# Performance work log

Hardware: AMD Instinct MI355X
Metric: run time of the kernel (lower is better)

Reference implementation:

```python
import jax, jax.numpy as jnp
import numpy as np

def setup_inputs() -> dict:
    key = jax.random.key(0)
    k1, k2, k3, k4 = jax.random.split(key, 4)
    B = 128
    x1 = jax.random.normal(k1, (B, 2048, 7, 7), dtype=jnp.float32)
    x2 = jax.random.normal(k2, (B, 2048, 7, 7), dtype=jnp.float32)
    x3 = jax.random.normal(k3, (B, 2048, 7, 7), dtype=jnp.float32)
    W = jax.random.normal(k4, (14, 2048), dtype=jnp.float32) * 0.02
    b = jnp.zeros((14,), dtype=jnp.float32)
    return {"x1": x1, "x2": x2, "x3": x3, "W": W, "b": b}

def reference(x1, x2, x3, W, b):
    B = x1.shape[0]
    # (B, 2048, 49)
    x1r = x1.reshape(B, 2048, 49)
    x2r = x2.reshape(B, 2048, 49)
    x3r = x3.reshape(B, 2048, 49)
    # diagonal of matmul(x3, x1^T) == per-row dot product over the 49-dim axis
    # (avoids materializing the (B,2048,2048) intermediate)
    d31 = jnp.einsum('bnc,bnc->bn', x3r, x1r)[..., None]  # (B, 2048, 1)
    d32 = jnp.einsum('bnc,bnc->bn', x3r, x2r)[..., None]
    # softmax over last (singleton) axis -> all ones, kept for faithfulness
    d31 = jax.nn.softmax(d31, axis=-1)
    d32 = jax.nn.softmax(d32, axis=-1)
    h = x1r + x1r * d31 + x2r * d32  # (B, 2048, 49)
    # AvgPool2d(7) on (B,2048,7,7) == mean over the 49 spatial positions
    feats = jnp.mean(h, axis=-1)  # (B, 2048)
    # dropout omitted (deterministic eval); fc
    logits = feats @ W.T + b  # (B, 14)
    return (logits, feats)
```

## Files before the change

kernel.cpp:

```cpp
#include <hip/hip_runtime.h>


#define FC_B 128
#define FC_N 2048
#define FC_J 14
#define TILE_ROWS 64
#define TILE_F (TILE_ROWS * 49)
#define TILE_V (TILE_F / 4)
#define TPB 4
#define RPB (TPB * TILE_ROWS)
#define NBLK (FC_B * FC_N / RPB)
#define BPB (FC_N / RPB)

__global__ __launch_bounds__(256) void fused_kernel(
    const float* __restrict__ x1, const float* __restrict__ x2,
    const float* __restrict__ W,
    float* __restrict__ feats, float* __restrict__ part)
{
    const int tid = threadIdx.x;
    __shared__ float buf[2][TILE_F];
    __shared__ __align__(16) float sf[RPB];

    const float4* q1 = (const float4*)x1 + (size_t)blockIdx.x * (TPB * TILE_V);
    const float4* q2 = (const float4*)x2 + (size_t)blockIdx.x * (TPB * TILE_V);

    float4 r1a, r1b, r1c, r2a, r2b, r2c, tl1, tl2;

    r1a = q1[tid]; r1b = q1[tid + 256]; r1c = q1[tid + 512];
    r2a = q2[tid]; r2b = q2[tid + 256]; r2c = q2[tid + 512];
    if (tid < 16) { tl1 = q1[768 + tid]; tl2 = q2[768 + tid]; }

    const int row = tid >> 2;
    const int tt = tid & 3;

    #pragma unroll
    for (int t = 0; t < TPB; ++t) {
        float4* smv = (float4*)buf[t & 1];
        float4 w0, w1, w2;
        w0.x = 2.f*r1a.x + r2a.x; w0.y = 2.f*r1a.y + r2a.y;
        w0.z = 2.f*r1a.z + r2a.z; w0.w = 2.f*r1a.w + r2a.w;
        w1.x = 2.f*r1b.x + r2b.x; w1.y = 2.f*r1b.y + r2b.y;
        w1.z = 2.f*r1b.z + r2b.z; w1.w = 2.f*r1b.w + r2b.w;
        w2.x = 2.f*r1c.x + r2c.x; w2.y = 2.f*r1c.y + r2c.y;
        w2.z = 2.f*r1c.z + r2c.z; w2.w = 2.f*r1c.w + r2c.w;
        smv[tid] = w0; smv[tid + 256] = w1; smv[tid + 512] = w2;
        if (tid < 16) {
            float4 wt;
            wt.x = 2.f*tl1.x + tl2.x; wt.y = 2.f*tl1.y + tl2.y;
            wt.z = 2.f*tl1.z + tl2.z; wt.w = 2.f*tl1.w + tl2.w;
            smv[768 + tid] = wt;
        }

        if (t < TPB - 1) {
            const float4* Q1 = q1 + (t + 1) * TILE_V;
            const float4* Q2 = q2 + (t + 1) * TILE_V;
            r1a = Q1[tid]; r1b = Q1[tid + 256]; r1c = Q1[tid + 512];
            r2a = Q2[tid]; r2b = Q2[tid + 256]; r2c = Q2[tid + 512];
            if (tid < 16) { tl1 = Q1[768 + tid]; tl2 = Q2[768 + tid]; }
        }

        asm volatile("s_waitcnt lgkmcnt(0)" ::: "memory");
        __builtin_amdgcn_s_barrier();

        const float* rp = buf[t & 1] + row * 49;
        float v = 0.f;
        #pragma unroll
        for (int k = 0; k < 12; ++k)
            v += rp[tt + 4 * k];
        if (tt == 0) v += rp[48];
        v += __shfl_xor(v, 1, 4);
        v += __shfl_xor(v, 2, 4);
        if (tt == 0) sf[t * TILE_ROWS + row] = v * (1.0f / 49.0f);
    }

    asm volatile("s_waitcnt lgkmcnt(0)" ::: "memory");
    __builtin_amdgcn_s_barrier();

    if (tid < 64)
        ((float4*)(feats + (size_t)blockIdx.x * RPB))[tid] =
            ((const float4*)sf)[tid];

    if (tid < 224) {
        const int j = tid >> 4;
        const int s = tid & 15;
        const int bb = blockIdx.x >> 3;
        const int blkin = blockIdx.x & (BPB - 1);
        const float* wrow = W + j * FC_N + blkin * RPB;
        float acc = 0.f;
        #pragma unroll
        for (int k = 0; k < 16; ++k)
            acc += sf[s + 16 * k] * wrow[s + 16 * k];
        acc += __shfl_xor(acc, 1, 16);
        acc += __shfl_xor(acc, 2, 16);
        acc += __shfl_xor(acc, 4, 16);
        acc += __shfl_xor(acc, 8, 16);
        if (s == 0)
            part[((bb * FC_J + j) << 3) + blkin] = acc;
    }
}

__global__ __launch_bounds__(256) void gather_kernel(const float* __restrict__ part,
                                                     const float* __restrict__ bias,
                                                     float* __restrict__ logits) {
    const int idx = blockIdx.x * 256 + threadIdx.x;
    if (idx >= FC_B * FC_J) return;
    const float4 p0 = ((const float4*)(part + ((size_t)idx << 3)))[0];
    const float4 p1 = ((const float4*)(part + ((size_t)idx << 3)))[1];
    logits[idx] = p0.x + p0.y + p0.z + p0.w
                + p1.x + p1.y + p1.z + p1.w + bias[idx % FC_J];
}

extern "C" void kernel_launch(void* const* d_in, const int* in_sizes, int n_in,
                              void* d_out, int out_size, void* d_ws, size_t ws_size,
                              hipStream_t stream) {
    const float* x1 = (const float*)d_in[0];
    const float* x2 = (const float*)d_in[1];
    const float* W = (const float*)d_in[3];
    const float* bias = (const float*)d_in[4];

    float* out = (float*)d_out;
    float* logits = out;
    float* feats = out + FC_B * FC_J;

    float* part = (float*)d_ws;

    fused_kernel<<<NBLK, 256, 0, stream>>>(x1, x2, W, feats, part);
    gather_kernel<<<(FC_B * FC_J + 255) / 256, 256, 0, stream>>>(part, bias, logits);
}
```

Measured before the change: 22.56 us.

## Give each wavefront a private sub-tile pipeline to drop block-wide barriers

Each of the four wavefronts now owns its own contiguous 64-row chunk and double-buffered LDS region. It processes that chunk in 16-row sub-tiles with a register prefetch issued before the current tile is consumed. The per-tile block barrier is replaced by a wave-local LDS wait, leaving a single __syncthreads before the FC epilogue. This is meant to remove barrier stalls and let waves stream memory independently, at the cost of more registers for the doubled prefetch buffers.

Measured after the change: 22.84 us. No clear change (+1.2%).

```diff
diff --git a/kernel.cpp b/kernel.cpp
--- a/kernel.cpp
+++ b/kernel.cpp
@@ -4,11 +4,12 @@
 #define FC_B 128
 #define FC_N 2048
 #define FC_J 14
-#define TILE_ROWS 64
-#define TILE_F (TILE_ROWS * 49)
-#define TILE_V (TILE_F / 4)
-#define TPB 4
-#define RPB (TPB * TILE_ROWS)
+#define SUBT 4
+#define SUB_ROWS 16
+#define SUB_F (SUB_ROWS * 49)
+#define SUB_V (SUB_F / 4)
+#define WCHUNK_V (SUBT * SUB_V)
+#define RPB 256
 #define NBLK (FC_B * FC_N / RPB)
 #define BPB (FC_N / RPB)
 
@@ -18,63 +19,67 @@
     float* __restrict__ feats, float* __restrict__ part)
 {
     const int tid = threadIdx.x;
-    __shared__ float buf[2][TILE_F];
+    const int w = tid >> 6;
+    const int lane = tid & 63;
+    __shared__ float buf[4][2][SUB_F];
     __shared__ __align__(16) float sf[RPB];
 
-    const float4* q1 = (const float4*)x1 + (size_t)blockIdx.x * (TPB * TILE_V);
-    const float4* q2 = (const float4*)x2 + (size_t)blockIdx.x * (TPB * TILE_V);
+    const float4* q1 = (const float4*)x1
+                     + (size_t)blockIdx.x * (RPB * 49 / 4) + w * WCHUNK_V;
+    const float4* q2 = (const float4*)x2
+                     + (size_t)blockIdx.x * (RPB * 49 / 4) + w * WCHUNK_V;
 
-    float4 r1a, r1b, r1c, r2a, r2b, r2c, tl1, tl2;
+    float4 a0[2], a1[2], a2[2], at[2], c0[2], c1[2], c2[2], ct[2];
 
-    r1a = q1[tid]; r1b = q1[tid + 256]; r1c = q1[tid + 512];
-    r2a = q2[tid]; r2b = q2[tid + 256]; r2c = q2[tid + 512];
-    if (tid < 16) { tl1 = q1[768 + tid]; tl2 = q2[768 + tid]; }
+    a0[0] = q1[lane]; a1[0] = q1[lane + 64]; a2[0] = q1[lane + 128];
+    c0[0] = q2[lane]; c1[0] = q2[lane + 64]; c2[0] = q2[lane + 128];
+    if (lane < 4) { at[0] = q1[192 + lane]; ct[0] = q2[192 + lane]; }
 
-    const int row = tid >> 2;
-    const int tt = tid & 3;
+    const int r = lane >> 2;
+    const int t4 = lane & 3;
 
     #pragma unroll
-    for (int t = 0; t < TPB; ++t) {
-        float4* smv = (float4*)buf[t & 1];
-        float4 w0, w1, w2;
-        w0.x = 2.f*r1a.x + r2a.x; w0.y = 2.f*r1a.y + r2a.y;
-        w0.z = 2.f*r1a.z + r2a.z; w0.w = 2.f*r1a.w + r2a.w;
-        w1.x = 2.f*r1b.x + r2b.x; w1.y = 2.f*r1b.y + r2b.y;
-        w1.z = 2.f*r1b.z + r2b.z; w1.w = 2.f*r1b.w + r2b.w;
-        w2.x = 2.f*r1c.x + r2c.x; w2.y = 2.f*r1c.y + r2c.y;
-        w2.z = 2.f*r1c.z + r2c.z; w2.w = 2.f*r1c.w + r2c.w;
-        smv[tid] = w0; smv[tid + 256] = w1; smv[tid + 512] = w2;
-        if (tid < 16) {
-            float4 wt;
-            wt.x = 2.f*tl1.x + tl2.x; wt.y = 2.f*tl1.y + tl2.y;
-            wt.z = 2.f*tl1.z + tl2.z; wt.w = 2.f*tl1.w + tl2.w;
-            smv[768 + tid] = wt;
+    for (int s = 0; s < SUBT; ++s) {
+        const int cur = s & 1, nxt = cur ^ 1;
+
+        if (s < SUBT - 1) {
+            const float4* Q1 = q1 + (s + 1) * SUB_V;
+            const float4* Q2 = q2 + (s + 1) * SUB_V;
+            a0[nxt] = Q1[lane]; a1[nxt] = Q1[lane + 64]; a2[nxt] = Q1[lane + 128];
+            c0[nxt] = Q2[lane]; c1[nxt] = Q2[lane + 64]; c2[nxt] = Q2[lane + 128];
+            if (lane < 4) { at[nxt] = Q1[192 + lane]; ct[nxt] = Q2[192 + lane]; }
         }
 
-        if (t < TPB - 1) {
-            const float4* Q1 = q1 + (t + 1) * TILE_V;
-            const float4* Q2 = q2 + (t + 1) * TILE_V;
-            r1a = Q1[tid]; r1b = Q1[tid + 256]; r1c = Q1[tid + 512];
-            r2a = Q2[tid]; r2b = Q2[tid + 256]; r2c = Q2[tid + 512];
-            if (tid < 16) { tl1 = Q1[768 + tid]; tl2 = Q2[768 + tid]; }
+        float4* smv = (float4*)buf[w][cur];
+        float4 w0, w1, w2;
+        w0.x = 2.f*a0[cur].x + c0[cur].x; w0.y = 2.f*a0[cur].y + c0[cur].y;
+        w0.z = 2.f*a0[cur].z + c0[cur].z; w0.w = 2.f*a0[cur].w + c0[cur].w;
+        w1.x = 2.f*a1[cur].x + c1[cur].x; w1.y = 2.f*a1[cur].y + c1[cur].y;
+        w1.z = 2.f*a1[cur].z + c1[cur].z; w1.w = 2.f*a1[cur].w + c1[cur].w;
+        w2.x = 2.f*a2[cur].x + c2[cur].x; w2.y = 2.f*a2[cur].y + c2[cur].y;
+        w2.z = 2.f*a2[cur].z + c2[cur].z; w2.w = 2.f*a2[cur].w + c2[cur].w;
+        smv[lane] = w0; smv[lane + 64] = w1; smv[lane + 128] = w2;
+        if (lane < 4) {
+            float4 wt;
+            wt.x = 2.f*at[cur].x + ct[cur].x; wt.y = 2.f*at[cur].y + ct[cur].y;
+            wt.z = 2.f*at[cur].z + ct[cur].z; wt.w = 2.f*at[cur].w + ct[cur].w;
+            smv[192 + lane] = wt;
         }
 
         asm volatile("s_waitcnt lgkmcnt(0)" ::: "memory");
-        __builtin_amdgcn_s_barrier();
 
-        const float* rp = buf[t & 1] + row * 49;
+        const float* rp = buf[w][cur] + r * 49;
         float v = 0.f;
         #pragma unroll
         for (int k = 0; k < 12; ++k)
-            v += rp[tt + 4 * k];
-        if (tt == 0) v += rp[48];
+            v += rp[t4 + 4 * k];
+        if (t4 == 0) v += rp[48];
         v += __shfl_xor(v, 1, 4);
         v += __shfl_xor(v, 2, 4);
-        if (tt == 0) sf[t * TILE_ROWS + row] = v * (1.0f / 49.0f);
+        if (t4 == 0) sf[w * 64 + s * SUB_ROWS + r] = v * (1.0f / 49.0f);
     }
 
-    asm volatile("s_waitcnt lgkmcnt(0)" ::: "memory");
-    __builtin_amdgcn_s_barrier();
+    __syncthreads();
 
     if (tid < 64)
         ((float4*)(feats + (size_t)blockIdx.x * RPB))[tid] =
@@ -82,19 +87,19 @@
 
     if (tid < 224) {
         const int j = tid >> 4;
-        const int s = tid & 15;
+        const int s16 = tid & 15;
         const int bb = blockIdx.x >> 3;
         const int blkin = blockIdx.x & (BPB - 1);
         const float* wrow = W + j * FC_N + blkin * RPB;
         float acc = 0.f;
         #pragma unroll
         for (int k = 0; k < 16; ++k)
-            acc += sf[s + 16 * k] * wrow[s + 16 * k];
+            acc += sf[s16 + 16 * k] * wrow[s16 + 16 * k];
         acc += __shfl_xor(acc, 1, 16);
         acc += __shfl_xor(acc, 2, 16);
         acc += __shfl_xor(acc, 4, 16);
         acc += __shfl_xor(acc, 8, 16);
-        if (s == 0)
+        if (s16 == 0)
             part[((bb * FC_J + j) << 3) + blkin] = acc;
     }
 }
```
